# Optimization experiments

Hardware: AMD Instinct MI355X
Metric: run time of the kernel (lower is better)

The kernel has to match this reference:

```python
import jax, jax.numpy as jnp
import numpy as np

MARGIN = 1.0

def setup_inputs() -> dict:
    key = jax.random.key(0)
    k1, k2, k3 = jax.random.split(key, 3)
    B, C, D = 65536, 1000, 512
    x = jax.random.normal(k1, (B, D), dtype=jnp.float32)
    x = x / jnp.linalg.norm(x, axis=1, keepdims=True)  # docstring: ||x||2 = 1
    labels = jax.random.randint(k2, (B,), 0, C, dtype=jnp.int64)
    centers = jax.random.normal(k3, (C, D), dtype=jnp.float32)
    return {"x": x, "labels": labels, "centers": centers}

def reference(x, labels, centers):
    # l2Norm applied to the centers (module is only used when l2Norm is truthy)
    c = centers / jnp.linalg.norm(centers, axis=1, keepdims=True)  # (C, D)
    # cosine distance to every center: one batched GEMM instead of per-sample loop
    dist = 1.0 - jnp.einsum("bd,cd->bc", x, c)                      # (B, C)
    pos = jnp.take_along_axis(dist, labels[:, None], axis=1)[:, 0]  # (B,)
    # min over all classes != label: mask own class with +inf
    same = jnp.arange(c.shape[0])[None, :] == labels[:, None]       # (B, C)
    neg = jnp.min(jnp.where(same, jnp.inf, dist), axis=1)           # (B,)
    # sum of per-sample hinge losses divided by batch size == mean
    return jnp.mean(jax.nn.relu(pos + MARGIN - neg))
```

## Files before the change

kernel.cpp:

```cpp
#include <hip/hip_runtime.h>
#include <stdint.h>

typedef short v8s __attribute__((ext_vector_type(8)));
typedef short v4s __attribute__((ext_vector_type(4)));
typedef float v4f __attribute__((ext_vector_type(4)));

#define BM 128
#define BN 128
#define BK 64
#define POS_INF __builtin_inff()

typedef __attribute__((address_space(3))) unsigned int lds_uint;
typedef const __attribute__((address_space(1))) unsigned int glb_uint;

__device__ __forceinline__ void load16_lds(const void* g, void* l) {
    __builtin_amdgcn_global_load_lds((glb_uint*)g, (lds_uint*)l, 16, 0, 0);
}

__device__ __forceinline__ short f2bf(float f) {
    uint32_t u = __builtin_bit_cast(uint32_t, f);
    u += 0x7fffu + ((u >> 16) & 1u);
    return (short)(u >> 16);
}

__global__ void prep(const float* __restrict__ centers,
                     unsigned short* __restrict__ cbf,
                     int C, int D, int CP, int CB,
                     const float* __restrict__ x,
                     unsigned short* __restrict__ xbf, size_t nx,
                     float* __restrict__ out) {
    const int b = blockIdx.x;
    const int t = threadIdx.x;
    if (b == 0 && t == 0) out[0] = 0.0f;
    if (b < CB) {
        const int wave = t >> 6, lane = t & 63;
        const int row = b * 4 + wave;
        if (row >= CP) return;
        if (row >= C) {
            v4s z = {0, 0, 0, 0};
            for (int d = lane * 4; d < D; d += 256)
                *(v4s*)&cbf[(size_t)row * D + d] = z;
            return;
        }
        const float* src = centers + (size_t)row * D;
        float ss = 0.0f;
        for (int d = lane * 4; d < D; d += 256) {
            v4f f = *(const v4f*)&src[d];
            ss += f.x * f.x + f.y * f.y + f.z * f.z + f.w * f.w;
        }
        #pragma unroll
        for (int off = 32; off; off >>= 1) ss += __shfl_xor(ss, off, 64);
        const float rn = rsqrtf(ss);
        for (int d = lane * 4; d < D; d += 256) {
            v4f f = *(const v4f*)&src[d];
            v4s s;
            s.x = f2bf(f.x * rn); s.y = f2bf(f.y * rn);
            s.z = f2bf(f.z * rn); s.w = f2bf(f.w * rn);
            *(v4s*)&cbf[(size_t)row * D + d] = s;
        }
    } else {
        const size_t i = ((size_t)(b - CB) * 256 + t) * 8;
        if (i >= nx) return;
        v4f f0 = *(const v4f*)&x[i];
        v4f f1 = *(const v4f*)&x[i + 4];
        v8s s;
        s[0] = f2bf(f0.x); s[1] = f2bf(f0.y); s[2] = f2bf(f0.z); s[3] = f2bf(f0.w);
        s[4] = f2bf(f1.x); s[5] = f2bf(f1.y); s[6] = f2bf(f1.z); s[7] = f2bf(f1.w);
        *(v8s*)&xbf[i] = s;
    }
}

__global__ void gemm_fused(const float* __restrict__ xf,
                           const unsigned short* __restrict__ xbf, int useBf,
                           const unsigned short* __restrict__ cbf,
                           const int* __restrict__ labels,
                           float* __restrict__ pos, float* __restrict__ partial,
                           int Bt, int C, int D, int NT) {
    __shared__ short As[BM * BK];
    __shared__ short Bs[BN * BK];

    const int t   = threadIdx.x;
    const int bid = blockIdx.x;
    const int xcd = bid & 7;
    const int per = bid >> 3;
    const int rowblk = (per >> 3) * 8 + xcd;
    const int nt     = per & 7;
    const int row0 = rowblk * BM;
    const int n0   = nt * BN;

    const int lane = t & 63;
    const int wave = t >> 6;
    const int wm = wave >> 1, wn = wave & 1;
    const int l15 = lane & 15, q = lane >> 4;

    const int rsub = lane >> 3;
    const int csrc = (lane & 7) ^ rsub;

    v4f acc[4][4];
    #pragma unroll
    for (int i = 0; i < 4; ++i)
        #pragma unroll
        for (int j = 0; j < 4; ++j)
            acc[i][j] = (v4f){0.f, 0.f, 0.f, 0.f};

    const int KT = D / BK;
    for (int kk = 0; kk < KT; ++kk) {
        const int k0 = kk * BK;
        #pragma unroll
        for (int p = 0; p < 4; ++p) {
            const int rbase = wave * 32 + p * 8;
            const unsigned short* g =
                &cbf[(size_t)(n0 + rbase + rsub) * D + k0 + csrc * 8];
            load16_lds(g, &Bs[rbase * BK]);
        }
        if (useBf) {
            #pragma unroll
            for (int p = 0; p < 4; ++p) {
                const int rbase = wave * 32 + p * 8;
                const unsigned short* g =
                    &xbf[(size_t)(row0 + rbase + rsub) * D + k0 + csrc * 8];
                load16_lds(g, &As[rbase * BK]);
            }
        } else {
            #pragma unroll
            for (int p = 0; p < 4; ++p) {
                const int r = (t >> 3) + p * 32;
                const int cs = t & 7;
                const float* src = &xf[(size_t)(row0 + r) * D + k0 + cs * 8];
                v4f f0 = *(const v4f*)&src[0];
                v4f f1 = *(const v4f*)&src[4];
                v8s s;
                s[0] = f2bf(f0.x); s[1] = f2bf(f0.y);
                s[2] = f2bf(f0.z); s[3] = f2bf(f0.w);
                s[4] = f2bf(f1.x); s[5] = f2bf(f1.y);
                s[6] = f2bf(f1.z); s[7] = f2bf(f1.w);
                *(v8s*)&As[r * BK + (cs ^ (r & 7)) * 8] = s;
            }
        }
        __syncthreads();
        #pragma unroll
        for (int ki = 0; ki < BK; ki += 32) {
            const int cbase = ki >> 3;
            v8s a[4], b[4];
            #pragma unroll
            for (int i = 0; i < 4; ++i) {
                const int m = wm * 64 + i * 16 + l15;
                a[i] = *(const v8s*)&As[m * BK + (((cbase + q) ^ (l15 & 7)) * 8)];
            }
            #pragma unroll
            for (int j = 0; j < 4; ++j) {
                const int n = wn * 64 + j * 16 + l15;
                b[j] = *(const v8s*)&Bs[n * BK + (((cbase + q) ^ (l15 & 7)) * 8)];
            }
            #pragma unroll
            for (int i = 0; i < 4; ++i)
                #pragma unroll
                for (int j = 0; j < 4; ++j)
                    acc[i][j] = __builtin_amdgcn_mfma_f32_16x16x32_bf16(
                        a[i], b[j], acc[i][j], 0, 0, 0);
        }
        __syncthreads();
    }

    int*   Ls    = (int*)As;
    float* sMinW = (float*)Bs;
    if (t < BM) Ls[t] = labels[row0 + t];
    __syncthreads();

    #pragma unroll
    for (int i = 0; i < 4; ++i) {
        #pragma unroll
        for (int rg = 0; rg < 4; ++rg) {
            const int row_l = wm * 64 + i * 16 + q * 4 + rg;
            const int lab = Ls[row_l];
            float m = POS_INF;
            #pragma unroll
            for (int j = 0; j < 4; ++j) {
                const int col = n0 + wn * 64 + j * 16 + l15;
                const float d = 1.0f - acc[i][j][rg];
                if (col == lab) pos[row0 + row_l] = d;
                else if (col < C) m = fminf(m, d);
            }
            m = fminf(m, __shfl_xor(m, 1, 64));
            m = fminf(m, __shfl_xor(m, 2, 64));
            m = fminf(m, __shfl_xor(m, 4, 64));
            m = fminf(m, __shfl_xor(m, 8, 64));
            if (l15 == 0) sMinW[wn * BM + row_l] = m;
        }
    }
    __syncthreads();
    if (t < BM) {
        const float m = fminf(sMinW[t], sMinW[BM + t]);
        partial[(size_t)nt * Bt + row0 + t] = m;
    }
}

__global__ void reduce_loss(const float* __restrict__ pos,
                            const float* __restrict__ partial,
                            int Bt, int NT, float margin,
                            float* __restrict__ out) {
    const int r = blockIdx.x * 256 + threadIdx.x;
    float h = 0.0f;
    if (r < Bt) {
        float neg = POS_INF;
        for (int tt = 0; tt < NT; ++tt)
            neg = fminf(neg, partial[(size_t)tt * Bt + r]);
        h = fmaxf(0.0f, pos[r] + margin - neg);
    }
    #pragma unroll
    for (int off = 32; off; off >>= 1) h += __shfl_down(h, off, 64);
    __shared__ float wsum[4];
    const int lane = threadIdx.x & 63, wave = threadIdx.x >> 6;
    if (lane == 0) wsum[wave] = h;
    __syncthreads();
    if (threadIdx.x == 0)
        atomicAdd(out, (wsum[0] + wsum[1] + wsum[2] + wsum[3]) * (1.0f / (float)Bt));
}

extern "C" void kernel_launch(void* const* d_in, const int* in_sizes, int n_in,
                              void* d_out, int out_size, void* d_ws, size_t ws_size,
                              hipStream_t stream) {
    const float* x       = (const float*)d_in[0];
    const int*   labels  = (const int*)d_in[1];
    const float* centers = (const float*)d_in[2];
    float* out = (float*)d_out;

    const int Bt = in_sizes[1];
    const int D  = in_sizes[0] / Bt;
    const int C  = in_sizes[2] / D;
    const int NT = (C + BN - 1) / BN;
    const int CP = NT * BN;
    const int NB = Bt / BM;

    char* ws = (char*)d_ws;
    unsigned short* cbf = (unsigned short*)ws;
    size_t off = (size_t)CP * D * 2;
    off = (off + 255) & ~(size_t)255;
    float* pos = (float*)(ws + off);      off += (size_t)Bt * 4;
    float* partial = (float*)(ws + off);  off += (size_t)NT * Bt * 4;
    unsigned short* xbf = (unsigned short*)(ws + off);
    const size_t needBig = off + (size_t)Bt * D * 2;
    const int useBf = (ws_size >= needBig) ? 1 : 0;

    const size_t nx = (size_t)Bt * D;
    const int CB = CP / 4;
    const int XB = useBf ? (int)((nx / 8 + 255) / 256) : 0;
    prep<<<CB + XB, 256, 0, stream>>>(centers, cbf, C, D, CP, CB, x, xbf, nx, out);

    gemm_fused<<<NB * NT, 256, 0, stream>>>(x, xbf, useBf, cbf, labels, pos,
                                            partial, Bt, C, D, NT);
    reduce_loss<<<(Bt + 255) / 256, 256, 0, stream>>>(pos, partial, Bt, NT, 1.0f, out);
}
```

Measured before the change: 290.3 us.

## Fuse loss reduction into GEMM via last-block counter and use 32x32 MFMA

Replaces the separate reduce kernel with a per-row-block arrival counter: the last column tile to finish for a row block computes the hinge loss and atomically adds to the output. The GEMM inner loop switches from 16x16x32 to 32x32x16 bf16 MFMA with 2x2 accumulators, which cuts LDS fragment loads per MFMA. Launch bounds of 4 waves-groups per CU are added. The counters are zeroed in the prep kernel, and atomics/fences add some synchronization cost.

```diff
diff --git a/kernel.cpp b/kernel.cpp
--- a/kernel.cpp
+++ b/kernel.cpp
@@ -4,6 +4,7 @@
 typedef short v8s __attribute__((ext_vector_type(8)));
 typedef short v4s __attribute__((ext_vector_type(4)));
 typedef float v4f __attribute__((ext_vector_type(4)));
+typedef float v16f __attribute__((ext_vector_type(16)));
 
 #define BM 128
 #define BN 128
@@ -28,11 +29,14 @@
                      int C, int D, int CP, int CB,
                      const float* __restrict__ x,
                      unsigned short* __restrict__ xbf, size_t nx,
+                     int* __restrict__ cnt, int NB,
                      float* __restrict__ out) {
     const int b = blockIdx.x;
     const int t = threadIdx.x;
     if (b == 0 && t == 0) out[0] = 0.0f;
     if (b < CB) {
+        const int g = b * 256 + t;
+        if (g < NB) cnt[g] = 0;
         const int wave = t >> 6, lane = t & 63;
         const int row = b * 4 + wave;
         if (row >= CP) return;
@@ -70,14 +74,18 @@
     }
 }
 
-__global__ void gemm_fused(const float* __restrict__ xf,
-                           const unsigned short* __restrict__ xbf, int useBf,
-                           const unsigned short* __restrict__ cbf,
-                           const int* __restrict__ labels,
-                           float* __restrict__ pos, float* __restrict__ partial,
-                           int Bt, int C, int D, int NT) {
-    __shared__ short As[BM * BK];
-    __shared__ short Bs[BN * BK];
+__global__ void __launch_bounds__(256, 4)
+gemm_fused(const float* __restrict__ xf,
+           const unsigned short* __restrict__ xbf, int useBf,
+           const unsigned short* __restrict__ cbf,
+           const int* __restrict__ labels,
+           float* __restrict__ pos, float* __restrict__ partial,
+           int* __restrict__ cnt,
+           int Bt, int C, int D, int NT, float margin,
+           float* __restrict__ out) {
+    __shared__ short LDSbuf[2 * BM * BK];
+    short* As = LDSbuf;
+    short* Bs = LDSbuf + BM * BK;
 
     const int t   = threadIdx.x;
     const int bid = blockIdx.x;
@@ -91,17 +99,19 @@
     const int lane = t & 63;
     const int wave = t >> 6;
     const int wm = wave >> 1, wn = wave & 1;
-    const int l15 = lane & 15, q = lane >> 4;
+    const int l31 = lane & 31, h = lane >> 5;
 
     const int rsub = lane >> 3;
     const int csrc = (lane & 7) ^ rsub;
 
-    v4f acc[4][4];
+    v16f acc[2][2];
     #pragma unroll
-    for (int i = 0; i < 4; ++i)
-        #pragma unroll
-        for (int j = 0; j < 4; ++j)
-            acc[i][j] = (v4f){0.f, 0.f, 0.f, 0.f};
+    for (int i = 0; i < 2; ++i)
+        #pragma unroll
+        for (int j = 0; j < 2; ++j)
+            #pragma unroll
+            for (int r = 0; r < 16; ++r)
+                acc[i][j][r] = 0.0f;
 
     const int KT = D / BK;
     for (int kk = 0; kk < KT; ++kk) {
@@ -139,24 +149,24 @@
         }
         __syncthreads();
         #pragma unroll
-        for (int ki = 0; ki < BK; ki += 32) {
-            const int cbase = ki >> 3;
-            v8s a[4], b[4];
-            #pragma unroll
-            for (int i = 0; i < 4; ++i) {
-                const int m = wm * 64 + i * 16 + l15;
-                a[i] = *(const v8s*)&As[m * BK + (((cbase + q) ^ (l15 & 7)) * 8)];
-            }
-            #pragma unroll
-            for (int j = 0; j < 4; ++j) {
-                const int n = wn * 64 + j * 16 + l15;
-                b[j] = *(const v8s*)&Bs[n * BK + (((cbase + q) ^ (l15 & 7)) * 8)];
-            }
-            #pragma unroll
-            for (int i = 0; i < 4; ++i)
+        for (int ks = 0; ks < 4; ++ks) {
+            const int chunk = ks * 2 + h;
+            v8s a[2], b[2];
+            #pragma unroll
+            for (int i = 0; i < 2; ++i) {
+                const int m = wm * 64 + i * 32 + l31;
+                a[i] = *(const v8s*)&As[m * BK + ((chunk ^ (m & 7)) * 8)];
+            }
+            #pragma unroll
+            for (int j = 0; j < 2; ++j) {
+                const int n = wn * 64 + j * 32 + l31;
+                b[j] = *(const v8s*)&Bs[n * BK + ((chunk ^ (n & 7)) * 8)];
+            }
+            #pragma unroll
+            for (int i = 0; i < 2; ++i)
                 #pragma unroll
-                for (int j = 0; j < 4; ++j)
-                    acc[i][j] = __builtin_amdgcn_mfma_f32_16x16x32_bf16(
+                for (int j = 0; j < 2; ++j)
+                    acc[i][j] = __builtin_amdgcn_mfma_f32_32x32x16_bf16(
                         a[i], b[j], acc[i][j], 0, 0, 0);
         }
         __syncthreads();
@@ -164,56 +174,71 @@
 
     int*   Ls    = (int*)As;
     float* sMinW = (float*)Bs;
+    int*   sLast = (int*)(Bs + 2 * BM * 2);
+    float* wsum  = (float*)(sLast + 1);
     if (t < BM) Ls[t] = labels[row0 + t];
     __syncthreads();
 
     #pragma unroll
-    for (int i = 0; i < 4; ++i) {
-        #pragma unroll
-        for (int rg = 0; rg < 4; ++rg) {
-            const int row_l = wm * 64 + i * 16 + q * 4 + rg;
+    for (int i = 0; i < 2; ++i) {
+        #pragma unroll
+        for (int rg = 0; rg < 16; ++rg) {
+            const int row_l = wm * 64 + i * 32 + (rg & 3) + 8 * (rg >> 2) + 4 * h;
             const int lab = Ls[row_l];
             float m = POS_INF;
             #pragma unroll
-            for (int j = 0; j < 4; ++j) {
-                const int col = n0 + wn * 64 + j * 16 + l15;
+            for (int j = 0; j < 2; ++j) {
+                const int col = n0 + wn * 64 + j * 32 + l31;
                 const float d = 1.0f - acc[i][j][rg];
-                if (col == lab) pos[row0 + row_l] = d;
+                if (col == lab)
+                    __hip_atomic_store(&pos[row0 + row_l], d,
+                                       __ATOMIC_RELAXED, __HIP_MEMORY_SCOPE_AGENT);
                 else if (col < C) m = fminf(m, d);
             }
             m = fminf(m, __shfl_xor(m, 1, 64));
             m = fminf(m, __shfl_xor(m, 2, 64));
             m = fminf(m, __shfl_xor(m, 4, 64));
             m = fminf(m, __shfl_xor(m, 8, 64));
-            if (l15 == 0) sMinW[wn * BM + row_l] = m;
+            m = fminf(m, __shfl_xor(m, 16, 64));
+            if (l31 == 0) sMinW[wn * BM + row_l] = m;
         }
     }
     __syncthreads();
     if (t < BM) {
         const float m = fminf(sMinW[t], sMinW[BM + t]);
-        partial[(size_t)nt * Bt + row0 + t] = m;
-    }
-}
-
-__global__ void reduce_loss(const float* __restrict__ pos,
-                            const float* __restrict__ partial,
-                            int Bt, int NT, float margin,
-                            float* __restrict__ out) {
-    const int r = blockIdx.x * 256 + threadIdx.x;
-    float h = 0.0f;
-    if (r < Bt) {
+        __hip_atomic_store(&partial[(size_t)nt * Bt + row0 + t], m,
+                           __ATOMIC_RELAXED, __HIP_MEMORY_SCOPE_AGENT);
+        __threadfence();
+    }
+    __syncthreads();
+
+    if (t == 0) {
+        const int old = __hip_atomic_fetch_add(&cnt[rowblk], 1,
+                                               __ATOMIC_ACQ_REL,
+                                               __HIP_MEMORY_SCOPE_AGENT);
+        *sLast = (old == NT - 1);
+    }
+    __syncthreads();
+    if (!*sLast) return;
+
+    __threadfence();
+    float hng = 0.0f;
+    if (t < BM) {
+        const int r = row0 + t;
         float neg = POS_INF;
         for (int tt = 0; tt < NT; ++tt)
-            neg = fminf(neg, partial[(size_t)tt * Bt + r]);
-        h = fmaxf(0.0f, pos[r] + margin - neg);
+            neg = fminf(neg, __hip_atomic_load(&partial[(size_t)tt * Bt + r],
+                                               __ATOMIC_RELAXED,
+                                               __HIP_MEMORY_SCOPE_AGENT));
+        const float p = __hip_atomic_load(&pos[r], __ATOMIC_RELAXED,
+                                          __HIP_MEMORY_SCOPE_AGENT);
+        hng = fmaxf(0.0f, p + margin - neg);
     }
     #pragma unroll
-    for (int off = 32; off; off >>= 1) h += __shfl_down(h, off, 64);
-    __shared__ float wsum[4];
-    const int lane = threadIdx.x & 63, wave = threadIdx.x >> 6;
-    if (lane == 0) wsum[wave] = h;
-    __syncthreads();
-    if (threadIdx.x == 0)
+    for (int off = 32; off; off >>= 1) hng += __shfl_down(hng, off, 64);
+    if (lane == 0) wsum[wave] = hng;
+    __syncthreads();
+    if (t == 0)
         atomicAdd(out, (wsum[0] + wsum[1] + wsum[2] + wsum[3]) * (1.0f / (float)Bt));
 }
 
@@ -238,6 +263,8 @@
     off = (off + 255) & ~(size_t)255;
     float* pos = (float*)(ws + off);      off += (size_t)Bt * 4;
     float* partial = (float*)(ws + off);  off += (size_t)NT * Bt * 4;
+    int* cnt = (int*)(ws + off);          off += (size_t)NB * 4;
+    off = (off + 255) & ~(size_t)255;
     unsigned short* xbf = (unsigned short*)(ws + off);
     const size_t needBig = off + (size_t)Bt * D * 2;
     const int useBf = (ws_size >= needBig) ? 1 : 0;
@@ -245,9 +272,9 @@
     const size_t nx = (size_t)Bt * D;
     const int CB = CP / 4;
     const int XB = useBf ? (int)((nx / 8 + 255) / 256) : 0;
-    prep<<<CB + XB, 256, 0, stream>>>(centers, cbf, C, D, CP, CB, x, xbf, nx, out);
+    prep<<<CB + XB, 256, 0, stream>>>(centers, cbf, C, D, CP, CB, x, xbf, nx,
+                                      cnt, NB, out);
 
     gemm_fused<<<NB * NT, 256, 0, stream>>>(x, xbf, useBf, cbf, labels, pos,
-                                            partial, Bt, C, D, NT);
-    reduce_loss<<<(Bt + 255) / 256, 256, 0, stream>>>(pos, partial, Bt, NT, 1.0f, out);
-}
+                                            partial, cnt, Bt, C, D, NT, 1.0f, out);
+}
```

Result: slower. 513.4 us (+76.8%).
